# Kernel tuning notes

Measured on AMD Instinct MI355X. Metric: run time of the kernel, lower is better.

The kernel has to match this reference:

```python
import jax, jax.numpy as jnp
from jax import lax
import numpy as np

H = W = 256          # resolution
HS, WS = 256, 8      # window: H_sp = H, W_sp = split_size (idx=0)
HEADS = 4
FF = 3.0             # focusing factor
EPS = 1e-6


def dwconv(x, w, b, pad):
    # depthwise conv, x: (B, C, h, w), w: (C, 1, k, k)
    y = lax.conv_general_dilated(x, w, (1, 1), [(pad, pad), (pad, pad)],
                                 dimension_numbers=('NCHW', 'OIHW', 'NCHW'),
                                 feature_group_count=x.shape[1])
    return y + b[None, :, None, None]


def _focus(t, scale):
    # ReLU feature map + focusing power, norm-preserving rescale
    t = jax.nn.relu(t) + EPS
    t = t / scale
    n0 = jnp.linalg.norm(t, axis=-1, keepdims=True)
    t = t ** FF
    return t / jnp.linalg.norm(t, axis=-1, keepdims=True) * n0


def setup_inputs() -> dict:
    key = jax.random.key(0)
    ks = jax.random.split(key, 7)
    C = 64
    hd = C // HEADS
    return {
        'x': jax.random.normal(ks[0], (4, H * W, C), dtype=jnp.float32),
        'w_qkv': jax.random.normal(ks[1], (3 * C, C), dtype=jnp.float32) * 0.05,
        'w_getv': jax.random.normal(ks[2], (C, 1, 3, 3), dtype=jnp.float32) * 0.1,
        'b_getv': jax.random.normal(ks[3], (C,), dtype=jnp.float32) * 0.01,
        'w_dwc': jax.random.normal(ks[4], (hd, 1, 5, 5), dtype=jnp.float32) * 0.1,
        'b_dwc': jax.random.normal(ks[5], (hd,), dtype=jnp.float32) * 0.01,
        'scale_param': jax.random.normal(ks[6], (1, 1, C), dtype=jnp.float32) * 0.1,
    }


def reference(x, w_qkv, w_getv, b_getv, w_dwc, b_dwc, scale_param):
    B, L, C = x.shape
    hd = C // HEADS
    n = HS * WS
    # qkv projection (1x1 conv == per-token linear, no bias)
    qkv = jnp.einsum('blc,dc->bld', x, w_qkv)
    q, k, v = jnp.split(qkv, 3, axis=-1)

    def win(t):  # img2windows: (B, L, C) -> (B*nw, n, C)
        t = t.transpose(0, 2, 1).reshape(B, C, H, W)
        t = t.reshape(B, C, H // HS, HS, W // WS, WS).transpose(0, 2, 4, 3, 5, 1)
        return t.reshape(-1, n, C)

    qw, kw = win(q), win(k)

    # v windows + LePE (3x3 depthwise conv per window)
    vimg = v.transpose(0, 2, 1).reshape(B, C, H, W)
    vimg = vimg.reshape(B, C, H // HS, HS, W // WS, WS).transpose(0, 2, 4, 1, 3, 5).reshape(-1, C, HS, WS)
    Bp = vimg.shape[0]
    lepe = dwconv(vimg, w_getv, b_getv, 1)
    lepe = lepe.reshape(Bp * HEADS, hd, n).transpose(0, 2, 1)  # (B'h, n, hd)
    vw = vimg.reshape(Bp, C, n).transpose(0, 2, 1)             # (B', n, C)

    scale = jax.nn.softplus(scale_param)
    qw = _focus(qw, scale)
    kw = _focus(kw, scale)

    def heads(t):  # (B', n, C) -> (B'h, n, hd)
        return t.reshape(Bp, n, HEADS, hd).transpose(0, 2, 1, 3).reshape(Bp * HEADS, n, hd)

    qh, kh, vh = heads(qw), heads(kw), heads(vw)

    # linear attention: z normalizer, kv aggregation
    z = 1.0 / (jnp.einsum('bic,bc->bi', qh, kh.sum(axis=1)) + EPS)
    kv = jnp.einsum('bjc,bjd->bcd', kh, vh)
    out = jnp.einsum('bic,bcd->bid', qh, kv) * z[..., None]

    # depthwise-conv feature map on v (5x5 per head)
    fmap = vh.transpose(0, 2, 1).reshape(Bp * HEADS, hd, HS, WS)
    fmap = dwconv(fmap, w_dwc, b_dwc, w_dwc.shape[-1] // 2)
    fmap = fmap.reshape(Bp * HEADS, hd, n).transpose(0, 2, 1)

    out = out + fmap + lepe
    # merge heads, windows back to image
    out = out.reshape(Bp, HEADS, n, hd).transpose(0, 2, 1, 3).reshape(Bp, n, C)
    out = out.reshape(B, H // HS, W // WS, HS, WS, C).transpose(0, 1, 3, 2, 4, 5).reshape(B, H * W, C)
    return out
```

## Files before the change

kernel.cpp:

```cpp
#include <hip/hip_runtime.h>


typedef float f32x4 __attribute__((ext_vector_type(4)));
typedef short bf8v  __attribute__((ext_vector_type(8)));
typedef short bf4v  __attribute__((ext_vector_type(4)));
typedef unsigned short u16;

#define MFMA __builtin_amdgcn_mfma_f32_16x16x32_bf16

static __device__ __forceinline__ u16 f2bf(float f){
  union { float f; unsigned int i; } v; v.f = f;
  return (u16)((v.i + 0x7FFFu + ((v.i >> 16) & 1u)) >> 16);
}
static __device__ __forceinline__ float bf2f(u16 u){
  union { unsigned int i; float f; } v; v.i = ((unsigned int)u) << 16; return v.f;
}
template<int CTRL>
static __device__ __forceinline__ float dppadd(float x){
  int m = __builtin_amdgcn_update_dpp(0, __builtin_bit_cast(int, x), CTRL, 0xF, 0xF, true);
  return x + __builtin_bit_cast(float, m);
}
static __device__ __forceinline__ float rowsum16(float x){
  x = dppadd<0x121>(x); x = dppadd<0x122>(x); x = dppadd<0x124>(x); x = dppadd<0x128>(x);
  return x;
}

static __device__ __forceinline__ void focus16(const f32x4 d[4], const float isc[4], float kh[4][4]){
  float s2[4] = {0,0,0,0}, s6[4] = {0,0,0,0};
#pragma unroll
  for (int nb = 0; nb < 4; ++nb)
#pragma unroll
    for (int r = 0; r < 4; ++r){
      float t = fmaxf(d[nb][r], 0.0f) + 1e-6f;
      t *= isc[nb];
      const float t2 = t * t;
      s2[r] += t2; s6[r] += t2 * t2 * t2;
      kh[nb][r] = t;
    }
#pragma unroll
  for (int r = 0; r < 4; ++r){
    const float f = sqrtf(rowsum16(s2[r]) / rowsum16(s6[r]));
#pragma unroll
    for (int nb = 0; nb < 4; ++nb){
      const float t = kh[nb][r];
      kh[nb][r] = t * t * t * f;
    }
  }
}

constexpr size_t NKV_OFF = 0;
constexpr size_t NKS_OFF = 4194304;
constexpr size_t NQF_OFF = 4325376;
constexpr size_t NV_OFF  = 37880064;
constexpr size_t NW_OFF  = 71434496;
constexpr size_t NWS_NEED  = 71434496;
constexpr size_t NWS_NEED2 = 71483648;

constexpr int A_XSH = 0;
constexpr int A_XSL = 16384;
constexpr int A_KFT = 32768;
constexpr int A_VTT = 49152;
constexpr int A_TOT = 65536;

constexpr int K_XSH = 0;
constexpr int K_XSL = 16384;
constexpr int K_KFT = 0;
constexpr int K_VTT = 16384;
constexpr int K_WH  = 32768;
constexpr int K_WL  = 57344;
constexpr int K_TOT = 81920;

__global__ __launch_bounds__(512, 8)
void nk0(const float* __restrict__ wqkv, float* __restrict__ ws)
{
  u16* wsp = (u16*)((char*)ws + NW_OFF);
  const int e = blockIdx.x * 512 + threadIdx.x;
  const float f = wqkv[e];
  const u16 hb = f2bf(f);
  wsp[e]         = hb;
  wsp[12288 + e] = f2bf(f - bf2f(hb));
}

template<bool PRE>
__global__ __launch_bounds__(512, 4)
void nk1(const float* __restrict__ xg, const float* __restrict__ wqkv,
         const float* __restrict__ scalep, float* __restrict__ ws)
{
  __shared__ __attribute__((aligned(16))) char smem[K_TOT];
  const int bid = blockIdx.x;
  const int qt = bid >> 7, wp = bid & 127;
  const int wcol = (wp & 31) * 8;
  const int tid = threadIdx.x, wv = tid >> 6, lane = tid & 63;
  const int g4 = lane >> 4, c15 = lane & 15;
  const size_t xbase = (size_t)(wp >> 5) * (65536ull * 64ull);
  const int swz = (c15 & 7) << 4;

  u16* qf_ws = (u16*)((char*)ws + NQF_OFF);
  u16* v_ws  = (u16*)((char*)ws + NV_OFF);

  if (bid == 0 && tid < 16){
    bf8v z8 = {0,0,0,0,0,0,0,0};
    *(bf8v*)(qf_ws + 262144ull*64ull + tid*8) = z8;
  }

  float isc[4];
#pragma unroll
  for (int nb = 0; nb < 4; ++nb) isc[nb] = 1.0f / logf(1.0f + expf(scalep[nb*16 + c15]));

  auto ldsplit = [&](const float* p, bf8v& hi, bf8v& lo){
    f32x4 u = *(const f32x4*)p;
    f32x4 w = *(const f32x4*)(p + 4);
#pragma unroll
    for (int j = 0; j < 4; ++j){
      u16 hb = f2bf(u[j]); hi[j]   = (short)hb; lo[j]   = (short)f2bf(u[j] - bf2f(hb));
      u16 hc = f2bf(w[j]); hi[4+j] = (short)hc; lo[4+j] = (short)f2bf(w[j] - bf2f(hc));
    }
  };

  if constexpr (PRE){
    const u16* wsp = (const u16*)((const char*)ws + NW_OFF);
    for (int ci = tid; ci < 1536; ci += 512){
      const int row = ci >> 3, c8 = ci & 7;
      const int off = row*128 + ((c8 ^ (row & 7)) << 4);
      *(bf8v*)(smem + K_WH + off) = *(const bf8v*)(wsp + row*64 + c8*8);
      *(bf8v*)(smem + K_WL + off) = *(const bf8v*)(wsp + 12288 + row*64 + c8*8);
    }
  } else {
    for (int ci = tid; ci < 1536; ci += 512){
      const int row = ci >> 3, c8 = ci & 7;
      bf8v hi, lo;
      ldsplit(wqkv + (size_t)row*64 + c8*8, hi, lo);
      const int off = row*128 + ((c8 ^ (row & 7)) << 4);
      *(bf8v*)(smem + K_WH + off) = hi;
      *(bf8v*)(smem + K_WL + off) = lo;
    }
  }
  __syncthreads();

  auto loadA = [&](int t){
    const int row0 = qt*64 + t*16;
    for (int ci = tid; ci < 1024; ci += 512){
      const int te = ci >> 3, c8 = ci & 7;
      const float* p = xg + xbase + ((size_t)(row0 + (te >> 3)) * 256 + wcol + (te & 7)) * 64 + c8 * 8;
      bf8v vh, vl;
      f32x4 u = *(const f32x4*)p, w = *(const f32x4*)(p + 4);
#pragma unroll
      for (int j = 0; j < 4; ++j){
        u16 hb = f2bf(u[j]); vh[j]   = (short)hb; vl[j]   = (short)f2bf(u[j] - bf2f(hb));
        u16 hc = f2bf(w[j]); vh[4+j] = (short)hc; vl[4+j] = (short)f2bf(w[j] - bf2f(hc));
      }
      const int off = te * 128 + ((c8 ^ (te & 7)) << 4);
      *(bf8v*)(smem + K_XSH + off) = vh;
      *(bf8v*)(smem + K_XSL + off) = vl;
    }
  };
  auto rdA = [&](int plane, int tokbase, int cc) -> bf8v {
    const int te = tokbase + c15;
    return *(const bf8v*)(smem + plane + te * 128 + ((cc ^ (te & 7)) << 4));
  };

  int wofs = 0;
  auto gemm6 = [&](int row, bf8v a0, bf8v a1, bf8v a0l, bf8v a1l) -> f32x4 {
    const int rbase = row*128 + wofs;
    const int o0 = (( g4      ^ (row & 7)) << 4);
    const int o1 = (((g4 + 4) ^ (row & 7)) << 4);
    bf8v h0 = *(const bf8v*)(smem + K_WH + rbase + o0);
    bf8v h1 = *(const bf8v*)(smem + K_WH + rbase + o1);
    bf8v l0 = *(const bf8v*)(smem + K_WL + rbase + o0);
    bf8v l1 = *(const bf8v*)(smem + K_WL + rbase + o1);
    f32x4 acc = {0,0,0,0};
    acc = MFMA(a0,  h0, acc, 0,0,0);
    acc = MFMA(a0,  l0, acc, 0,0,0);
    acc = MFMA(a0l, h0, acc, 0,0,0);
    acc = MFMA(a1,  h1, acc, 0,0,0);
    acc = MFMA(a1,  l1, acc, 0,0,0);
    acc = MFMA(a1l, h1, acc, 0,0,0);
    return acc;
  };

  float ksA[4] = {0,0,0,0};
  f32x4 kvacc = {0,0,0,0};
  const int kvhead = wv >> 1, kvs0 = (wv & 1) * 2;

#pragma unroll 1
  for (int tile = 0; tile < 4; ++tile){
    asm volatile("" : "+v"(wofs));
    __syncthreads();
    loadA(tile);
    __syncthreads();

    bf8v a0  = rdA(K_XSH, wv*16, g4),  a1  = rdA(K_XSH, wv*16, 4 + g4);
    bf8v a0l = rdA(K_XSL, wv*16, g4),  a1l = rdA(K_XSL, wv*16, 4 + g4);
    __syncthreads();

    const int tglob = wp*2048 + qt*512 + tile*128 + wv*16 + 4*g4;
    const int tb2 = (wv*16 + 4*g4) * 2;

    f32x4 d4[4];
#pragma unroll
    for (int nb = 0; nb < 4; ++nb) d4[nb] = gemm6(64 + nb*16 + c15, a0, a1, a0l, a1l);
    float kh[4][4];
    focus16(d4, isc, kh);
#pragma unroll
    for (int nb = 0; nb < 4; ++nb){
      ksA[nb] += (kh[nb][0] + kh[nb][1]) + (kh[nb][2] + kh[nb][3]);
      bf4v pk;
#pragma unroll
      for (int r = 0; r < 4; ++r) pk[r] = (short)f2bf(kh[nb][r]);
      *(bf4v*)(smem + K_KFT + (nb*16 + c15)*256 + (tb2 ^ swz)) = pk;
    }

#pragma unroll
    for (int nb = 0; nb < 4; ++nb) d4[nb] = gemm6(nb*16 + c15, a0, a1, a0l, a1l);
    focus16(d4, isc, kh);
#pragma unroll
    for (int nb = 0; nb < 4; ++nb)
#pragma unroll
      for (int r = 0; r < 4; ++r)
        qf_ws[(size_t)(tglob + r)*64 + nb*16 + c15] = f2bf(kh[nb][r]);

#pragma unroll
    for (int nb = 0; nb < 4; ++nb){
      f32x4 acc = gemm6(128 + nb*16 + c15, a0, a1, a0l, a1l);
      bf4v pv;
#pragma unroll
      for (int r = 0; r < 4; ++r) pv[r] = (short)f2bf(acc[r]);
      *(bf4v*)(smem + K_VTT + (nb*16 + c15)*256 + (tb2 ^ swz)) = pv;
    }

    __syncthreads();

    {
      const int tbase = wp*2048 + qt*512 + tile*128;
      for (int ci = tid; ci < 1024; ci += 512){
        const int ch = ci >> 4, j = ci & 15;
        bf8v val = *(const bf8v*)(smem + K_VTT + ch*256 + ((j ^ (ch & 7)) << 4));
        *(bf8v*)(v_ws + (size_t)ch*262144 + tbase + j*8) = val;
      }
    }
#pragma unroll
    for (int s = 0; s < 2; ++s){
      const int tb = (kvs0 + s)*64 + g4*16;
      bf8v af = *(const bf8v*)(smem + K_KFT + (kvhead*16 + c15)*256 + (tb ^ swz));
      bf8v bv = *(const bf8v*)(smem + K_VTT + (kvhead*16 + c15)*256 + (tb ^ swz));
      kvacc = MFMA(af, bv, kvacc, 0,0,0);
    }
  }

  __syncthreads();
  float* ksp = (float*)smem;
#pragma unroll
  for (int nb = 0; nb < 4; ++nb) ksp[(wv*4 + g4)*64 + nb*16 + c15] = ksA[nb];
  float* kvp = (float*)((char*)ws + NKV_OFF) + ((size_t)(wp*4 + qt)*8 + wv) * 256;
#pragma unroll
  for (int r = 0; r < 4; ++r) kvp[(4*g4 + r)*16 + c15] = kvacc[r];
  __syncthreads();
  if (tid < 64){
    float s = 0.0f;
    for (int j = 0; j < 32; ++j) s += ksp[j*64 + tid];
    ((float*)((char*)ws + NKS_OFF))[(wp*4 + qt)*64 + tid] = s;
  }
}

constexpr int N_VT  = 0;
constexpr int N_ATT = 21504;
constexpr int N_KVB = 43008;
constexpr int N_CMB = 48128;
constexpr int N_KSH = 55040;
constexpr int N_ZZ  = 55296;
constexpr int N_TOT = 57344;

__global__ __launch_bounds__(512, 4)
void nk2(const float* __restrict__ wgetv, const float* __restrict__ bgetv,
         const float* __restrict__ wdwc,  const float* __restrict__ bdwc,
         const float* __restrict__ ws,    float* __restrict__ outg)
{
  __shared__ __attribute__((aligned(16))) char smem[N_TOT];
  const int bid = blockIdx.x;
  const int qt = bid >> 7, wp = bid & 127;
  const int wcol = (wp & 31) * 8;
  const int tid = threadIdx.x, wv = tid >> 6, lane = tid & 63;
  const int g4 = lane >> 4, c15 = lane & 15;
  const size_t xbase = (size_t)(wp >> 5) * (65536ull * 64ull);

  const u16*   qf_ws = (const u16*)((const char*)ws + NQF_OFF);
  const u16*   v_ws  = (const u16*)((const char*)ws + NV_OFF);
  const float* kv_ws = (const float*)((const char*)ws + NKV_OFF);
  const float* ks_ws = (const float*)((const char*)ws + NKS_OFF);
  u16*   vt   = (u16*)(smem + N_VT);
  u16*   att  = (u16*)(smem + N_ATT);
  u16*   kvb  = (u16*)(smem + N_KVB);
  float* cmb  = (float*)(smem + N_CMB);
  float* kshf = (float*)(smem + N_KSH);
  float* zz   = (float*)(smem + N_ZZ);

  for (int e = tid; e < 64*27; e += 512){
    const int ch = e / 27, i = e - ch*27;
    float v = 0.0f;
    if (i < 25){
      const int dy = i / 5, dx = i - dy*5;
      v = wdwc[(ch & 15)*25 + i];
      if (dy >= 1 && dy <= 3 && dx >= 1 && dx <= 3)
        v += wgetv[ch*9 + (dy-1)*3 + (dx-1)];
    } else if (i == 25){
      v = bdwc[ch & 15] + bgetv[ch];
    }
    cmb[e] = v;
  }
  if (tid < 64){
    float s = 0.0f;
#pragma unroll
    for (int q2 = 0; q2 < 4; ++q2) s += ks_ws[(wp*4 + q2)*64 + tid];
    kshf[tid] = s;
  }
  for (int e = tid; e < 2560; e += 512){
    const int h2 = e / 640, rem = e - h2*640, d = rem / 40, k = rem - d*40;
    u16 val = 0;
    if (k < 16){
      float s = 0.0f;
#pragma unroll
      for (int q2 = 0; q2 < 4; ++q2)
#pragma unroll
        for (int sl = 0; sl < 2; ++sl)
          s += kv_ws[((size_t)(wp*4 + q2)*8 + h2*2 + sl)*256 + k*16 + d];
      val = f2bf(s);
    }
    kvb[e] = val;
  }
  __syncthreads();

#pragma unroll 1
  for (int tile = 0; tile < 4; ++tile){
    const int tile_r0 = qt*64 + tile*16;
    const int t_base  = wp*2048 + qt*512 + tile*128;
    __syncthreads();

    for (int c = tid; c < 1280; c += 512){
      const int ch = c / 20, slot = c - ch*20;
      const int grow = tile_r0 - 2 + slot;
      bf8v val = {0,0,0,0,0,0,0,0};
      if ((unsigned)grow < 256u)
        val = *(const bf8v*)(v_ws + (size_t)ch*262144 + wp*2048 + grow*8);
      *(bf8v*)((char*)vt + ch*336 + slot*16) = val;
    }
    {
      const int tokL = tid >> 2, hz = tid & 3;
      const size_t qo = (size_t)(t_base + tokL)*64 + hz*16;
      bf8v qa = *(const bf8v*)(qf_ws + qo);
      bf8v qb = *(const bf8v*)(qf_ws + qo + 8);
      float dot = 0.0f;
#pragma unroll
      for (int j = 0; j < 8; ++j){
        dot += bf2f((u16)qa[j]) * kshf[hz*16 + j];
        dot += bf2f((u16)qb[j]) * kshf[hz*16 + 8 + j];
      }
      zz[hz*128 + tokL] = 1.0f / (dot + 1e-6f);
    }
    __syncthreads();

#pragma unroll
    for (int nb = 0; nb < 4; ++nb){
      bf8v aq = *(const bf8v*)(qf_ws + (size_t)(t_base + wv*16 + c15)*64 + nb*16 + g4*8);
      bf8v bq = *(const bf8v*)(kvb + nb*640 + c15*40 + g4*8);
      f32x4 dat = {0,0,0,0};
      dat = MFMA(aq, bq, dat, 0,0,0);
#pragma unroll
      for (int r = 0; r < 4; ++r){
        const int tokL = wv*16 + 4*g4 + r;
        att[tokL*84 + nb*16 + c15] = f2bf(dat[r] * zz[nb*128 + tokL]);
      }
    }
    __syncthreads();

    {
      const int ch = lane;
      float cb[26];
#pragma unroll
      for (int i = 0; i < 26; ++i) cb[i] = cmb[ch*27 + i];
      float rf[6][8];
#pragma unroll
      for (int j = 0; j < 6; ++j){
        bf8v rv = *(const bf8v*)((char*)vt + ch*336 + (wv*2 + j)*16);
#pragma unroll
        for (int i = 0; i < 8; ++i) rf[j][i] = bf2f((u16)rv[i]);
      }
#pragma unroll
      for (int o = 0; o < 2; ++o){
        float acc[8];
#pragma unroll
        for (int s = 0; s < 8; ++s) acc[s] = cb[25];
#pragma unroll
        for (int dy = 0; dy < 5; ++dy)
#pragma unroll
          for (int dx = 0; dx < 5; ++dx){
            const float w = cb[dy*5 + dx];
#pragma unroll
            for (int s = 0; s < 8; ++s){
              const int c = s + dx - 2;
              if (c >= 0 && c < 8) acc[s] += rf[o + dy][c] * w;
            }
          }
        const int tok0 = (wv*2 + o)*8;
        const size_t obase = xbase + ((size_t)(tile_r0 + wv*2 + o)*256 + wcol)*64 + ch;
#pragma unroll
        for (int s = 0; s < 8; ++s)
          outg[obase + (size_t)s*64] = acc[s] + bf2f(att[(tok0 + s)*84 + ch]);
      }
    }
  }
}

constexpr int    WS_KV = 0;
constexpr int    WS_KS = 524288;
constexpr size_t WS_NEED_BYTES = (524288ull + 32768ull) * 4ull;

__global__ __launch_bounds__(512, 2)
void fla_k1(const float* __restrict__ xg, const float* __restrict__ wqkv,
            const float* __restrict__ scalep, float* __restrict__ ws)
{
  __shared__ __attribute__((aligned(16))) char smem[A_TOT];
  const int bid = blockIdx.x;
  const int qt = bid >> 7, wp = bid & 127;
  const int b = wp >> 5, wcol = (wp & 31) * 8;
  const int tid = threadIdx.x, wv = tid >> 6, lane = tid & 63;
  const int g4 = lane >> 4, c15 = lane & 15;
  const size_t xbase = (size_t)b * (65536ull * 64ull);
  const int swz = (c15 & 7) << 4;

  auto ldsplit = [&](const float* p, bf8v& hi, bf8v& lo){
    f32x4 u = *(const f32x4*)p;
    f32x4 w = *(const f32x4*)(p + 4);
#pragma unroll
    for (int j = 0; j < 4; ++j){
      u16 hb = f2bf(u[j]); hi[j]   = (short)hb; lo[j]   = (short)f2bf(u[j] - bf2f(hb));
      u16 hc = f2bf(w[j]); hi[4+j] = (short)hc; lo[4+j] = (short)f2bf(w[j] - bf2f(hc));
    }
  };
  auto loadA = [&](int t){
    const int row0 = qt*64 + t*16;
    for (int ci = tid; ci < 1024; ci += 512){
      const int te = ci >> 3, c8 = ci & 7;
      const float* p = xg + xbase + ((size_t)(row0 + (te >> 3)) * 256 + wcol + (te & 7)) * 64 + c8 * 8;
      bf8v vh, vl;
      f32x4 u = *(const f32x4*)p, w = *(const f32x4*)(p + 4);
#pragma unroll
      for (int j = 0; j < 4; ++j){
        u16 hb = f2bf(u[j]); vh[j]   = (short)hb; vl[j]   = (short)f2bf(u[j] - bf2f(hb));
        u16 hc = f2bf(w[j]); vh[4+j] = (short)hc; vl[4+j] = (short)f2bf(w[j] - bf2f(hc));
      }
      const int off = te * 128 + ((c8 ^ (te & 7)) << 4);
      *(bf8v*)(smem + A_XSH + off) = vh;
      *(bf8v*)(smem + A_XSL + off) = vl;
    }
  };
  auto rdA = [&](int plane, int tokbase, int cc) -> bf8v {
    const int te = tokbase + c15;
    return *(const bf8v*)(smem + plane + te * 128 + ((cc ^ (te & 7)) << 4));
  };

  if (wv < 4){
    float isc[4];
#pragma unroll
    for (int nb = 0; nb < 4; ++nb) isc[nb] = 1.0f / logf(1.0f + expf(scalep[nb*16 + c15]));
    bf8v WKh[4][2], WKl[4][2];
#pragma unroll
    for (int nb = 0; nb < 4; ++nb)
#pragma unroll
      for (int kt = 0; kt < 2; ++kt)
        ldsplit(wqkv + (size_t)(64 + nb*16 + c15)*64 + kt*32 + 8*g4, WKh[nb][kt], WKl[nb][kt]);

    float ksA[4] = {0,0,0,0};
    f32x4 kvacc = {0,0,0,0};
    for (int t = 0; t < 4; ++t){
      __syncthreads();
      loadA(t);
      __syncthreads();
#pragma unroll
      for (int s = 0; s < 2; ++s){
        const int tg = wv*2 + s;
        bf8v a0  = rdA(A_XSH, tg*16, g4),  a1  = rdA(A_XSH, tg*16, 4 + g4);
        bf8v a0l = rdA(A_XSL, tg*16, g4),  a1l = rdA(A_XSL, tg*16, 4 + g4);
        f32x4 dk[4];
#pragma unroll
        for (int nb = 0; nb < 4; ++nb){
          f32x4 acc = {0,0,0,0};
          acc = MFMA(a0,  WKh[nb][0], acc, 0,0,0);
          acc = MFMA(a0,  WKl[nb][0], acc, 0,0,0);
          acc = MFMA(a0l, WKh[nb][0], acc, 0,0,0);
          acc = MFMA(a1,  WKh[nb][1], acc, 0,0,0);
          acc = MFMA(a1,  WKl[nb][1], acc, 0,0,0);
          acc = MFMA(a1l, WKh[nb][1], acc, 0,0,0);
          dk[nb] = acc;
        }
        float kh[4][4];
        focus16(dk, isc, kh);
        const int tb2 = (tg*16 + 4*g4) * 2;
#pragma unroll
        for (int nb = 0; nb < 4; ++nb){
          ksA[nb] += (kh[nb][0] + kh[nb][1]) + (kh[nb][2] + kh[nb][3]);
          bf4v pk;
#pragma unroll
          for (int r = 0; r < 4; ++r) pk[r] = (short)f2bf(kh[nb][r]);
          *(bf4v*)(smem + A_KFT + (nb*16 + c15)*256 + (tb2 ^ swz)) = pk;
        }
      }
      __syncthreads();
#pragma unroll
      for (int k2 = 0; k2 < 4; ++k2){
        const int tb = k2*64 + g4*16;
        bf8v af = *(const bf8v*)(smem + A_KFT + (wv*16 + c15)*256 + (tb ^ swz));
        bf8v bv = *(const bf8v*)(smem + A_VTT + (wv*16 + c15)*256 + (tb ^ swz));
        kvacc = MFMA(af, bv, kvacc, 0,0,0);
      }
    }
    __syncthreads();
    float* ksp = (float*)smem;
#pragma unroll
    for (int nb = 0; nb < 4; ++nb) ksp[(wv*4 + g4)*64 + nb*16 + c15] = ksA[nb];
    float* kvp = ws + WS_KV + ((wp*4 + qt)*4 + wv) * 256;
#pragma unroll
    for (int r = 0; r < 4; ++r) kvp[(4*g4 + r)*16 + c15] = kvacc[r];
  } else {
    bf8v WVh[4][2], WVl[4][2];
#pragma unroll
    for (int nb = 0; nb < 4; ++nb)
#pragma unroll
      for (int kt = 0; kt < 2; ++kt)
        ldsplit(wqkv + (size_t)(128 + nb*16 + c15)*64 + kt*32 + 8*g4, WVh[nb][kt], WVl[nb][kt]);

    for (int t = 0; t < 4; ++t){
      __syncthreads();
      loadA(t);
      __syncthreads();
#pragma unroll
      for (int s = 0; s < 2; ++s){
        const int tg = (wv - 4)*2 + s;
        bf8v a0  = rdA(A_XSH, tg*16, g4),  a1  = rdA(A_XSH, tg*16, 4 + g4);
        bf8v a0l = rdA(A_XSL, tg*16, g4),  a1l = rdA(A_XSL, tg*16, 4 + g4);
        const int tb2 = (tg*16 + 4*g4) * 2;
#pragma unroll
        for (int nb = 0; nb < 4; ++nb){
          f32x4 acc = {0,0,0,0};
          acc = MFMA(a0,  WVh[nb][0], acc, 0,0,0);
          acc = MFMA(a0,  WVl[nb][0], acc, 0,0,0);
          acc = MFMA(a0l, WVh[nb][0], acc, 0,0,0);
          acc = MFMA(a1,  WVh[nb][1], acc, 0,0,0);
          acc = MFMA(a1,  WVl[nb][1], acc, 0,0,0);
          acc = MFMA(a1l, WVh[nb][1], acc, 0,0,0);
          bf4v pv;
#pragma unroll
          for (int r = 0; r < 4; ++r) pv[r] = (short)f2bf(acc[r]);
          *(bf4v*)(smem + A_VTT + (nb*16 + c15)*256 + (tb2 ^ swz)) = pv;
        }
      }
      __syncthreads();
    }
    __syncthreads();
  }
  __syncthreads();
  if (tid < 64){
    const float* ksp = (const float*)smem;
    float s = 0.0f;
    for (int j = 0; j < 16; ++j) s += ksp[j*64 + tid];
    ws[WS_KS + (wp*4 + qt)*64 + tid] = s;
  }
}

constexpr int LDS_X   = 0;
constexpr int LDS_VT2 = 49152;
constexpr int LDS_QFM = 54528;
constexpr int LDS_KVB = 58624;
constexpr int LDS_KSH = 62976;
constexpr int LDS_TOT = 63040;

__global__ __launch_bounds__(512, 2)
void fla_k2(const float* __restrict__ xg,   const float* __restrict__ wqkv,
            const float* __restrict__ wgetv,const float* __restrict__ bgetv,
            const float* __restrict__ wdwc, const float* __restrict__ bdwc,
            const float* __restrict__ scalep, const float* __restrict__ ws,
            float* __restrict__ outg)
{
  __shared__ __attribute__((aligned(16))) char smem[LDS_TOT];
  u16*   xs  = (u16*)(smem + LDS_X);
  u16*   vt2 = (u16*)(smem + LDS_VT2);
  u16*   qfm = (u16*)(smem + LDS_QFM);
  u16*   kvB = (u16*)(smem + LDS_KVB);
  float* ksh = (float*)(smem + LDS_KSH);

  const int bid  = blockIdx.x;
  const int h    = bid >> 7;
  const int wp   = bid & 127;
  const int b    = wp >> 5;
  const int wcol = (wp & 31) * 8;
  const int tid  = threadIdx.x;
  const int wv   = tid >> 6;
  const int lane = tid & 63;
  const int g4   = lane >> 4;
  const int c15  = lane & 15;
  const size_t xbase = (size_t)b * (65536ull * 64ull);

  float isc[4];
#pragma unroll
  for (int nb = 0; nb < 4; ++nb){
    float p = scalep[nb*16 + c15];
    isc[nb] = 1.0f / logf(1.0f + expf(p));
  }
  auto ldsplit = [&](const float* p, bf8v& hi, bf8v& lo){
    f32x4 u = *(const f32x4*)p;
    f32x4 w = *(const f32x4*)(p + 4);
#pragma unroll
    for (int j = 0; j < 4; ++j){
      u16 hb = f2bf(u[j]); hi[j]   = (short)hb; lo[j]   = (short)f2bf(u[j] - bf2f(hb));
      u16 hc = f2bf(w[j]); hi[4+j] = (short)hc; lo[4+j] = (short)f2bf(w[j] - bf2f(hc));
    }
  };
  bf8v WVh[2], WVl[2];
#pragma unroll
  for (int kt = 0; kt < 2; ++kt)
    ldsplit(wqkv + (size_t)(128 + h*16 + c15)*64 + kt*32 + 8*g4, WVh[kt], WVl[kt]);

  auto load_x = [&](int row0, int nrows){
    const int total = nrows * 64;
    for (int ci = tid; ci < total; ci += 512){
      const int te = ci >> 3;
      const int c8 = ci & 7;
      const int hs = row0 + (te >> 3);
      bf8v vh = {0,0,0,0,0,0,0,0}, vl = {0,0,0,0,0,0,0,0};
      if (hs >= 0 && hs < 256){
        const size_t l = (size_t)hs * 256 + wcol + (te & 7);
        const float* p = xg + xbase + l*64 + c8*8;
        f32x4 u = *(const f32x4*)p;
        f32x4 w = *(const f32x4*)(p + 4);
#pragma unroll
        for (int j = 0; j < 4; ++j){
          u16 hb = f2bf(u[j]); vh[j]   = (short)hb; vl[j]   = (short)f2bf(u[j] - bf2f(hb));
          u16 hc = f2bf(w[j]); vh[4+j] = (short)hc; vl[4+j] = (short)f2bf(w[j] - bf2f(hc));
        }
      }
      const int off = te*128 + ((c8 ^ (te & 7)) << 4);
      *(bf8v*)((char*)xs + off)         = vh;
      *(bf8v*)((char*)xs + 20480 + off) = vl;
    }
  };
  auto read_af = [&](int rowbase, int kt, int plane) -> bf8v {
    const int te = rowbase + c15;
    const int cc = kt*4 + g4;
    return *(const bf8v*)((char*)xs + plane*20480 + te*128 + ((cc ^ (te & 7)) << 4));
  };
  auto focus = [&](const f32x4* dmat, float* fh){
    float s2[4] = {0,0,0,0}, s6[4] = {0,0,0,0};
    float h1[4], h2[4];
#pragma unroll
    for (int nb = 0; nb < 4; ++nb){
#pragma unroll
      for (int r = 0; r < 4; ++r){
        float t = fmaxf(dmat[nb][r], 0.0f) + 1e-6f;
        t *= isc[nb];
        float t2 = t * t;
        s2[r] += t2;
        s6[r] += t2 * t2 * t2;
        if (nb == h){ h1[r] = t; h2[r] = t2; }
      }
    }
#pragma unroll
    for (int r = 0; r < 4; ++r){
      float a2 = rowsum16(s2[r]);
      float a6 = rowsum16(s6[r]);
      float f  = sqrtf(a2 / a6);
      fh[r] = h1[r] * h2[r] * f;
    }
  };

  if (tid < 16){
    float s = 0.0f;
#pragma unroll
    for (int q2 = 0; q2 < 4; ++q2) s += ws[WS_KS + (wp*4 + q2)*64 + h*16 + tid];
    ksh[tid] = s;
  }
  {
    const int d = tid >> 5, k = tid & 31;
    float s = 0.0f;
    if (k < 16){
#pragma unroll
      for (int q2 = 0; q2 < 4; ++q2) s += ws[WS_KV + ((wp*4 + q2)*4 + h)*256 + k*16 + d];
    }
    kvB[d*40 + k] = (k < 16) ? f2bf(s) : (u16)0;
  }
  __syncthreads();

  const bf8v  kvfrag = *(const bf8v*)((char*)kvB + c15*80 + g4*16);
  const float ksr    = ksh[c15];

  bf8v WQh[4][2], WQl[4][2];
#pragma unroll
  for (int nb = 0; nb < 4; ++nb)
#pragma unroll
    for (int kt = 0; kt < 2; ++kt)
      ldsplit(wqkv + (size_t)(nb*16 + c15)*64 + kt*32 + 8*g4, WQh[nb][kt], WQl[nb][kt]);
  float wdw[25], wge[9];
#pragma unroll
  for (int i = 0; i < 25; ++i) wdw[i] = wdwc[c15*25 + i];
#pragma unroll
  for (int i = 0; i < 9;  ++i) wge[i] = wgetv[(h*16 + c15)*9 + i];
  const float bdw = bdwc[c15];
  const float bge = bgetv[h*16 + c15];

  for (int tile = 0; tile < 16; ++tile){
    __syncthreads();
    load_x(tile*16 - 2, 20);
    __syncthreads();

    for (int mt = wv; mt < 10; mt += 8){
      bf8v va0  = read_af(16*mt, 0, 0);
      bf8v va1  = read_af(16*mt, 1, 0);
      bf8v va0l = read_af(16*mt, 0, 1);
      bf8v va1l = read_af(16*mt, 1, 1);
      f32x4 dv = {0,0,0,0};
      dv = MFMA(va0,  WVh[0], dv, 0, 0, 0);
      dv = MFMA(va0,  WVl[0], dv, 0, 0, 0);
      dv = MFMA(va0l, WVh[0], dv, 0, 0, 0);
      dv = MFMA(va1,  WVh[1], dv, 0, 0, 0);
      dv = MFMA(va1,  WVl[1], dv, 0, 0, 0);
      dv = MFMA(va1l, WVh[1], dv, 0, 0, 0);
      const int te = 16*mt + 4*g4;
      bf4v pv;
#pragma unroll
      for (int r = 0; r < 4; ++r) pv[r] = (short)f2bf(dv[r]);
      *(bf4v*)((char*)vt2 + c15*336 + (te >> 3)*16 + (te & 7)*2) = pv;
    }

    bf8v a0  = read_af(16 + 16*wv, 0, 0);
    bf8v a1  = read_af(16 + 16*wv, 1, 0);
    bf8v a0l = read_af(16 + 16*wv, 0, 1);
    bf8v a1l = read_af(16 + 16*wv, 1, 1);
    f32x4 dq[4];
#pragma unroll
    for (int nb = 0; nb < 4; ++nb){
      f32x4 acc = {0,0,0,0};
      acc = MFMA(a0,  WQh[nb][0], acc, 0, 0, 0);
      acc = MFMA(a0,  WQl[nb][0], acc, 0, 0, 0);
      acc = MFMA(a0l, WQh[nb][0], acc, 0, 0, 0);
      acc = MFMA(a1,  WQh[nb][1], acc, 0, 0, 0);
      acc = MFMA(a1,  WQl[nb][1], acc, 0, 0, 0);
      acc = MFMA(a1l, WQh[nb][1], acc, 0, 0, 0);
      dq[nb] = acc;
    }
    float qh[4];
    focus(dq, qh);
    float z[4];
#pragma unroll
    for (int r = 0; r < 4; ++r){
      float dot = rowsum16(qh[r] * ksr);
      z[r] = 1.0f / (dot + 1e-6f);
    }
    {
      const int base = wv*512 + (c15 >> 3)*256 + (c15 & 7)*2;
#pragma unroll
      for (int r = 0; r < 4; ++r)
        *(u16*)((char*)qfm + base + (4*g4 + r)*16) = f2bf(qh[r]);
    }

    __syncthreads();

    bf8v aq = *(const bf8v*)((char*)qfm + wv*512 + (g4 & 1)*256 + c15*16);
    f32x4 dat = {0,0,0,0};
    dat = MFMA(aq, kvfrag, dat, 0, 0, 0);

    const int  hsl = 2*wv + (g4 >> 1);
    const bool w0  = ((g4 & 1) == 0);
    float swv[5][8];
#pragma unroll
    for (int dy = 0; dy < 5; ++dy){
      bf8v rv = *(const bf8v*)((char*)vt2 + c15*336 + (hsl + dy)*16);
      float rf[8];
#pragma unroll
      for (int i = 0; i < 8; ++i) rf[i] = bf2f((u16)rv[i]);
      swv[dy][0] = w0 ? 0.0f : rf[2];
      swv[dy][1] = w0 ? 0.0f : rf[3];
      swv[dy][2] = w0 ? rf[0] : rf[4];
      swv[dy][3] = w0 ? rf[1] : rf[5];
      swv[dy][4] = w0 ? rf[2] : rf[6];
      swv[dy][5] = w0 ? rf[3] : rf[7];
      swv[dy][6] = w0 ? rf[4] : 0.0f;
      swv[dy][7] = w0 ? rf[5] : 0.0f;
    }

#pragma unroll
    for (int r = 0; r < 4; ++r){
      float accf = bdw;
#pragma unroll
      for (int dy = 0; dy < 5; ++dy)
#pragma unroll
        for (int dx = 0; dx < 5; ++dx)
          accf += swv[dy][r + dx] * wdw[dy*5 + dx];
      float accl = bge;
#pragma unroll
      for (int ky = 0; ky < 3; ++ky)
#pragma unroll
        for (int kx = 0; kx < 3; ++kx)
          accl += swv[1 + ky][r + 1 + kx] * wge[ky*3 + kx];
      const int    twin = tile*128 + 16*wv + 4*g4 + r;
      const size_t l    = (size_t)(twin >> 3) * 256 + wcol + (twin & 7);
      outg[xbase + l*64 + h*16 + c15] = dat[r] * z[r] + accf + accl;
    }
  }
}

extern "C" void kernel_launch(void* const* d_in, const int* in_sizes, int n_in,
                              void* d_out, int out_size, void* d_ws, size_t ws_size,
                              hipStream_t stream)
{
  (void)in_sizes; (void)n_in; (void)out_size;
  const float* xg     = (const float*)d_in[0];
  const float* wqkv   = (const float*)d_in[1];
  const float* wgetv  = (const float*)d_in[2];
  const float* bgetv  = (const float*)d_in[3];
  const float* wdwc   = (const float*)d_in[4];
  const float* bdwc   = (const float*)d_in[5];
  const float* scalep = (const float*)d_in[6];
  float* out = (float*)d_out;
  float* ws  = (float*)d_ws;

  if (d_ws != nullptr && ws_size >= NWS_NEED2){
    nk0<<<dim3(24), dim3(512), 0, stream>>>(wqkv, ws);
    nk1<true><<<dim3(512), dim3(512), 0, stream>>>(xg, wqkv, scalep, ws);
    nk2<<<dim3(512), dim3(512), 0, stream>>>(wgetv, bgetv, wdwc, bdwc, ws, out);
  } else if (d_ws != nullptr && ws_size >= NWS_NEED){
    nk1<false><<<dim3(512), dim3(512), 0, stream>>>(xg, wqkv, scalep, ws);
    nk2<<<dim3(512), dim3(512), 0, stream>>>(wgetv, bgetv, wdwc, bdwc, ws, out);
  } else {
    fla_k1<<<dim3(512), dim3(512), 0, stream>>>(xg, wqkv, scalep, ws);
    fla_k2<<<dim3(512), dim3(512), 0, stream>>>(xg, wqkv, wgetv, bgetv, wdwc, bdwc, scalep, ws, out);
  }
}
```

Measured before the change: 94.76 us.

## Stage q features through LDS for coalesced stores/loads and split kv into hi/lo bf16

In nk1 the focused q features now go into a swizzled LDS tile and are then written to global memory as 16-byte coalesced vectors, replacing scattered 2-byte stores. In nk2 each q tile is loaded into LDS once with coalesced reads and shared by the z-normalizer and the MFMA, instead of each being read from global. The kv matrix is also split into hi and lo bf16 parts, giving two MFMAs for better accuracy. The cost is extra barriers, more LDS in nk2 (which may lower occupancy), an extra MFMA, and removal of the zero-padding write at the end of qf_ws.

Result: faster. 92.86 us (-2.0%).

```diff
diff --git a/kernel.cpp b/kernel.cpp
--- a/kernel.cpp
+++ b/kernel.cpp
@@ -66,6 +66,7 @@
 constexpr int K_XSL = 16384;
 constexpr int K_KFT = 0;
 constexpr int K_VTT = 16384;
+constexpr int K_QFS = 0;
 constexpr int K_WH  = 32768;
 constexpr int K_WL  = 57344;
 constexpr int K_TOT = 81920;
@@ -97,11 +98,6 @@
 
   u16* qf_ws = (u16*)((char*)ws + NQF_OFF);
   u16* v_ws  = (u16*)((char*)ws + NV_OFF);
-
-  if (bid == 0 && tid < 16){
-    bf8v z8 = {0,0,0,0,0,0,0,0};
-    *(bf8v*)(qf_ws + 262144ull*64ull + tid*8) = z8;
-  }
 
   float isc[4];
 #pragma unroll
@@ -195,6 +191,7 @@
 
     const int tglob = wp*2048 + qt*512 + tile*128 + wv*16 + 4*g4;
     const int tb2 = (wv*16 + 4*g4) * 2;
+    const int tbase = wp*2048 + qt*512 + tile*128;
 
     f32x4 d4[4];
 #pragma unroll
@@ -211,15 +208,6 @@
     }
 
 #pragma unroll
-    for (int nb = 0; nb < 4; ++nb) d4[nb] = gemm6(nb*16 + c15, a0, a1, a0l, a1l);
-    focus16(d4, isc, kh);
-#pragma unroll
-    for (int nb = 0; nb < 4; ++nb)
-#pragma unroll
-      for (int r = 0; r < 4; ++r)
-        qf_ws[(size_t)(tglob + r)*64 + nb*16 + c15] = f2bf(kh[nb][r]);
-
-#pragma unroll
     for (int nb = 0; nb < 4; ++nb){
       f32x4 acc = gemm6(128 + nb*16 + c15, a0, a1, a0l, a1l);
       bf4v pv;
@@ -230,13 +218,10 @@
 
     __syncthreads();
 
-    {
-      const int tbase = wp*2048 + qt*512 + tile*128;
-      for (int ci = tid; ci < 1024; ci += 512){
-        const int ch = ci >> 4, j = ci & 15;
-        bf8v val = *(const bf8v*)(smem + K_VTT + ch*256 + ((j ^ (ch & 7)) << 4));
-        *(bf8v*)(v_ws + (size_t)ch*262144 + tbase + j*8) = val;
-      }
+    for (int ci = tid; ci < 1024; ci += 512){
+      const int ch = ci >> 4, j = ci & 15;
+      bf8v val = *(const bf8v*)(smem + K_VTT + ch*256 + ((j ^ (ch & 7)) << 4));
+      *(bf8v*)(v_ws + (size_t)ch*262144 + tbase + j*8) = val;
     }
 #pragma unroll
     for (int s = 0; s < 2; ++s){
@@ -244,6 +229,27 @@
       bf8v af = *(const bf8v*)(smem + K_KFT + (kvhead*16 + c15)*256 + (tb ^ swz));
       bf8v bv = *(const bf8v*)(smem + K_VTT + (kvhead*16 + c15)*256 + (tb ^ swz));
       kvacc = MFMA(af, bv, kvacc, 0,0,0);
+    }
+    __syncthreads();
+
+#pragma unroll
+    for (int nb = 0; nb < 4; ++nb) d4[nb] = gemm6(nb*16 + c15, a0, a1, a0l, a1l);
+    focus16(d4, isc, kh);
+#pragma unroll
+    for (int nb = 0; nb < 4; ++nb)
+#pragma unroll
+      for (int r = 0; r < 4; ++r){
+        const int tokL = wv*16 + 4*g4 + r;
+        const int c8w = 2*nb + (c15 >> 3);
+        *(u16*)(smem + K_QFS + tokL*128 + ((c8w ^ (tokL & 7)) << 4) + (c15 & 7)*2)
+            = f2bf(kh[nb][r]);
+      }
+    __syncthreads();
+
+    for (int ci = tid; ci < 1024; ci += 512){
+      const int tok = ci >> 3, c8 = ci & 7;
+      bf8v val = *(const bf8v*)(smem + K_QFS + tok*128 + ((c8 ^ (tok & 7)) << 4));
+      *(bf8v*)(qf_ws + (size_t)(tbase + tok)*64 + c8*8) = val;
     }
   }
 
@@ -264,11 +270,13 @@
 
 constexpr int N_VT  = 0;
 constexpr int N_ATT = 21504;
-constexpr int N_KVB = 43008;
-constexpr int N_CMB = 48128;
-constexpr int N_KSH = 55040;
-constexpr int N_ZZ  = 55296;
-constexpr int N_TOT = 57344;
+constexpr int N_QF  = 43008;
+constexpr int N_KVH = 59392;
+constexpr int N_KVL = 64512;
+constexpr int N_CMB = 69632;
+constexpr int N_KSH = 76544;
+constexpr int N_ZZ  = 76800;
+constexpr int N_TOT = 78848;
 
 __global__ __launch_bounds__(512, 4)
 void nk2(const float* __restrict__ wgetv, const float* __restrict__ bgetv,
@@ -289,7 +297,6 @@
   const float* ks_ws = (const float*)((const char*)ws + NKS_OFF);
   u16*   vt   = (u16*)(smem + N_VT);
   u16*   att  = (u16*)(smem + N_ATT);
-  u16*   kvb  = (u16*)(smem + N_KVB);
   float* cmb  = (float*)(smem + N_CMB);
   float* kshf = (float*)(smem + N_KSH);
   float* zz   = (float*)(smem + N_ZZ);
@@ -315,7 +322,7 @@
   }
   for (int e = tid; e < 2560; e += 512){
     const int h2 = e / 640, rem = e - h2*640, d = rem / 40, k = rem - d*40;
-    u16 val = 0;
+    u16 vh = 0, vl = 0;
     if (k < 16){
       float s = 0.0f;
 #pragma unroll
@@ -323,9 +330,11 @@
 #pragma unroll
         for (int sl = 0; sl < 2; ++sl)
           s += kv_ws[((size_t)(wp*4 + q2)*8 + h2*2 + sl)*256 + k*16 + d];
-      val = f2bf(s);
-    }
-    kvb[e] = val;
+      vh = f2bf(s);
+      vl = f2bf(s - bf2f(vh));
+    }
+    ((u16*)(smem + N_KVH))[e] = vh;
+    ((u16*)(smem + N_KVL))[e] = vl;
   }
   __syncthreads();
 
@@ -343,11 +352,17 @@
         val = *(const bf8v*)(v_ws + (size_t)ch*262144 + wp*2048 + grow*8);
       *(bf8v*)((char*)vt + ch*336 + slot*16) = val;
     }
+    for (int ci = tid; ci < 1024; ci += 512){
+      const int tok = ci >> 3, c8 = ci & 7;
+      bf8v val = *(const bf8v*)(qf_ws + (size_t)(t_base + tok)*64 + c8*8);
+      *(bf8v*)(smem + N_QF + tok*128 + ((c8 ^ (tok & 7)) << 4)) = val;
+    }
+    __syncthreads();
+
     {
       const int tokL = tid >> 2, hz = tid & 3;
-      const size_t qo = (size_t)(t_base + tokL)*64 + hz*16;
-      bf8v qa = *(const bf8v*)(qf_ws + qo);
-      bf8v qb = *(const bf8v*)(qf_ws + qo + 8);
+      bf8v qa = *(const bf8v*)(smem + N_QF + tokL*128 + (((2*hz)     ^ (tokL & 7)) << 4));
+      bf8v qb = *(const bf8v*)(smem + N_QF + tokL*128 + (((2*hz + 1) ^ (tokL & 7)) << 4));
       float dot = 0.0f;
 #pragma unroll
       for (int j = 0; j < 8; ++j){
@@ -360,10 +375,14 @@
 
 #pragma unroll
     for (int nb = 0; nb < 4; ++nb){
-      bf8v aq = *(const bf8v*)(qf_ws + (size_t)(t_base + wv*16 + c15)*64 + nb*16 + g4*8);
-      bf8v bq = *(const bf8v*)(kvb + nb*640 + c15*40 + g4*8);
+      const int tokA = wv*16 + c15;
+      const int c8a  = (2*nb + g4) & 7;
+      bf8v aq = *(const bf8v*)(smem + N_QF + tokA*128 + ((c8a ^ (tokA & 7)) << 4));
+      bf8v bh = *(const bf8v*)(smem + N_KVH + nb*1280 + c15*80 + g4*16);
+      bf8v bl = *(const bf8v*)(smem + N_KVL + nb*1280 + c15*80 + g4*16);
       f32x4 dat = {0,0,0,0};
-      dat = MFMA(aq, bq, dat, 0,0,0);
+      dat = MFMA(aq, bh, dat, 0,0,0);
+      dat = MFMA(aq, bl, dat, 0,0,0);
 #pragma unroll
       for (int r = 0; r < 4; ++r){
         const int tokL = wv*16 + 4*g4 + r;
```
